# Optimization experiments

Measured on AMD Instinct MI355X. Metric: run time of the kernel, lower is better.

## Reference

```python
import jax, jax.numpy as jnp
import numpy as np

MAX_LORAS = 16
D_IN = 4096
D_OUT = 64
B = 32
S = 2048


def setup_inputs() -> dict:
    key = jax.random.key(0)
    k1, k2, k3 = jax.random.split(key, 3)
    x = jax.random.normal(k1, (B, S, D_IN), dtype=jnp.float32)
    adapter_ids = jax.random.randint(k2, (B,), 0, MAX_LORAS)
    # weight table: (max_loras, input_size, output_size) since memory_transpose=True
    weight = jax.random.normal(k3, (MAX_LORAS, D_IN, D_OUT), dtype=jnp.float32) * 0.02
    return {"x": x, "adapter_ids": adapter_ids, "weight": weight}


def reference(x, adapter_ids, weight):
    # get_weight: gather per-sample weight [B, D_IN, D_OUT]
    weights = weight[adapter_ids]
    # memory_transpose=True path: einsum('bij,bjk->bik')
    return jnp.einsum('bij,bjk->bik', x, weights)
```

## Files before the change

### kernel.cpp

```cpp
#include <hip/hip_runtime.h>

#define DIN 4096
#define DOUT 64
#define SEQ 2048
#define BK 64
#define WT_STRIDE 72

typedef __bf16 bf16x8 __attribute__((ext_vector_type(8)));
typedef float f32x4 __attribute__((ext_vector_type(4)));

__global__ __launch_bounds__(256, 2)
void lora_gemm_kernel(const float* __restrict__ x,
                      const int* __restrict__ adapter_ids,
                      const float* __restrict__ weight,
                      float* __restrict__ out)
{
    __shared__ __align__(16) __bf16 wt[64 * WT_STRIDE];

    const int bid  = blockIdx.x;
    const int row0 = bid * 64;
    const int b    = row0 / SEQ;
    const int aid  = adapter_ids[b];
    const float* wbase = weight + (size_t)aid * DIN * DOUT;

    const int tid  = threadIdx.x;
    const int wave = tid >> 6;
    const int lane = tid & 63;
    const int m16  = lane & 15;
    const int quad = lane >> 4;

    const float* xrow = x + (size_t)(row0 + wave * 16 + m16) * DIN + quad * 8;

    f32x4 acc[4];
#pragma unroll
    for (int t = 0; t < 4; ++t) acc[t] = (f32x4)0.0f;

    const int s_kk = tid >> 4;
    const int s_n4 = tid & 15;

    for (int k0 = 0; k0 < DIN; k0 += BK) {
#pragma unroll
        for (int p = 0; p < 4; ++p) {
            const int kk = p * 16 + s_kk;
            const f32x4 w4 = *(const f32x4*)(wbase + (size_t)(k0 + kk) * DOUT + s_n4 * 4);
#pragma unroll
            for (int i = 0; i < 4; ++i)
                wt[(s_n4 * 4 + i) * WT_STRIDE + kk] = (__bf16)w4[i];
        }
        __syncthreads();

#pragma unroll
        for (int ks = 0; ks < BK; ks += 32) {
            const f32x4 xa = *(const f32x4*)(xrow + k0 + ks);
            const f32x4 xb = *(const f32x4*)(xrow + k0 + ks + 4);
            bf16x8 a;
            a[0] = (__bf16)xa[0]; a[1] = (__bf16)xa[1];
            a[2] = (__bf16)xa[2]; a[3] = (__bf16)xa[3];
            a[4] = (__bf16)xb[0]; a[5] = (__bf16)xb[1];
            a[6] = (__bf16)xb[2]; a[7] = (__bf16)xb[3];
#pragma unroll
            for (int t = 0; t < 4; ++t) {
                const bf16x8 bf = *(const bf16x8*)(&wt[(t * 16 + m16) * WT_STRIDE + ks + quad * 8]);
                acc[t] = __builtin_amdgcn_mfma_f32_16x16x32_bf16(a, bf, acc[t], 0, 0, 0);
            }
        }
        __syncthreads();
    }

    float* obase = out + (size_t)(row0 + wave * 16 + quad * 4) * DOUT + m16;
#pragma unroll
    for (int i = 0; i < 4; ++i)
#pragma unroll
        for (int t = 0; t < 4; ++t)
            obase[(size_t)i * DOUT + t * 16] = acc[t][i];
}

extern "C" void kernel_launch(void* const* d_in, const int* in_sizes, int n_in,
                              void* d_out, int out_size, void* d_ws, size_t ws_size,
                              hipStream_t stream) {
    const float* x   = (const float*)d_in[0];
    const int*   ids = (const int*)d_in[1];
    const float* w   = (const float*)d_in[2];
    float* out = (float*)d_out;

    const int total_rows = 32 * SEQ;
    dim3 grid(total_rows / 64);
    dim3 block(256);
    lora_gemm_kernel<<<grid, block, 0, stream>>>(x, ids, w, out);
}
```

Before: 1.389 ms.

## Pre-transpose weights to bf16 and read B fragments directly from global

Adds a preprocessing kernel that converts all adapter weight tables to bf16 in an N-major (transposed) layout inside the workspace. The GEMM kernel then loads its B fragments straight from global/L2 memory, with no shared-memory staging and no __syncthreads per K tile, and occupancy is raised to 4 blocks per SM. This removes the per-block fp32 weight reload, conversion and LDS transpose, at the cost of an extra kernel launch and more global/L2 traffic for weight fragments.

New measurement: 1.499 ms. 1.08x slower.

```diff
diff --git a/kernel.cpp b/kernel.cpp
--- a/kernel.cpp
+++ b/kernel.cpp
@@ -3,25 +3,33 @@
 #define DIN 4096
 #define DOUT 64
 #define SEQ 2048
-#define BK 64
-#define WT_STRIDE 72
+#define NADPT 16
 
 typedef __bf16 bf16x8 __attribute__((ext_vector_type(8)));
 typedef float f32x4 __attribute__((ext_vector_type(4)));
 
-__global__ __launch_bounds__(256, 2)
+__global__ __launch_bounds__(256)
+void transpose_w_kernel(const float* __restrict__ w, __bf16* __restrict__ wT)
+{
+    const int a  = blockIdx.y;
+    const int k0 = blockIdx.x * 32 + (threadIdx.x >> 6) * 8;
+    const int n  = threadIdx.x & 63;
+    const float* src = w + ((size_t)a * DIN + k0) * DOUT + n;
+    bf16x8 v;
+#pragma unroll
+    for (int j = 0; j < 8; ++j)
+        v[j] = (__bf16)src[(size_t)j * DOUT];
+    *(bf16x8*)(wT + ((size_t)a * DOUT + n) * DIN + k0) = v;
+}
+
+__global__ __launch_bounds__(256, 4)
 void lora_gemm_kernel(const float* __restrict__ x,
                       const int* __restrict__ adapter_ids,
-                      const float* __restrict__ weight,
+                      const __bf16* __restrict__ wT,
                       float* __restrict__ out)
 {
-    __shared__ __align__(16) __bf16 wt[64 * WT_STRIDE];
-
-    const int bid  = blockIdx.x;
-    const int row0 = bid * 64;
-    const int b    = row0 / SEQ;
-    const int aid  = adapter_ids[b];
-    const float* wbase = weight + (size_t)aid * DIN * DOUT;
+    const int row0 = blockIdx.x * 64;
+    const int aid  = adapter_ids[row0 / SEQ];
 
     const int tid  = threadIdx.x;
     const int wave = tid >> 6;
@@ -29,42 +37,27 @@
     const int m16  = lane & 15;
     const int quad = lane >> 4;
 
-    const float* xrow = x + (size_t)(row0 + wave * 16 + m16) * DIN + quad * 8;
+    const float*  xrow = x  + (size_t)(row0 + wave * 16 + m16) * DIN + quad * 8;
+    const __bf16* wb   = wT + ((size_t)aid * DOUT + m16) * DIN + quad * 8;
 
     f32x4 acc[4];
 #pragma unroll
     for (int t = 0; t < 4; ++t) acc[t] = (f32x4)0.0f;
 
-    const int s_kk = tid >> 4;
-    const int s_n4 = tid & 15;
-
-    for (int k0 = 0; k0 < DIN; k0 += BK) {
+#pragma unroll 2
+    for (int k = 0; k < DIN; k += 32) {
+        const f32x4 xa = *(const f32x4*)(xrow + k);
+        const f32x4 xb = *(const f32x4*)(xrow + k + 4);
+        bf16x8 a;
+        a[0] = (__bf16)xa[0]; a[1] = (__bf16)xa[1];
+        a[2] = (__bf16)xa[2]; a[3] = (__bf16)xa[3];
+        a[4] = (__bf16)xb[0]; a[5] = (__bf16)xb[1];
+        a[6] = (__bf16)xb[2]; a[7] = (__bf16)xb[3];
 #pragma unroll
-        for (int p = 0; p < 4; ++p) {
-            const int kk = p * 16 + s_kk;
-            const f32x4 w4 = *(const f32x4*)(wbase + (size_t)(k0 + kk) * DOUT + s_n4 * 4);
-#pragma unroll
-            for (int i = 0; i < 4; ++i)
-                wt[(s_n4 * 4 + i) * WT_STRIDE + kk] = (__bf16)w4[i];
+        for (int t = 0; t < 4; ++t) {
+            const bf16x8 bf = *(const bf16x8*)(wb + (size_t)t * 16 * DIN + k);
+            acc[t] = __builtin_amdgcn_mfma_f32_16x16x32_bf16(a, bf, acc[t], 0, 0, 0);
         }
-        __syncthreads();
-
-#pragma unroll
-        for (int ks = 0; ks < BK; ks += 32) {
-            const f32x4 xa = *(const f32x4*)(xrow + k0 + ks);
-            const f32x4 xb = *(const f32x4*)(xrow + k0 + ks + 4);
-            bf16x8 a;
-            a[0] = (__bf16)xa[0]; a[1] = (__bf16)xa[1];
-            a[2] = (__bf16)xa[2]; a[3] = (__bf16)xa[3];
-            a[4] = (__bf16)xb[0]; a[5] = (__bf16)xb[1];
-            a[6] = (__bf16)xb[2]; a[7] = (__bf16)xb[3];
-#pragma unroll
-            for (int t = 0; t < 4; ++t) {
-                const bf16x8 bf = *(const bf16x8*)(&wt[(t * 16 + m16) * WT_STRIDE + ks + quad * 8]);
-                acc[t] = __builtin_amdgcn_mfma_f32_16x16x32_bf16(a, bf, acc[t], 0, 0, 0);
-            }
-        }
-        __syncthreads();
     }
 
     float* obase = out + (size_t)(row0 + wave * 16 + quad * 4) * DOUT + m16;
@@ -82,9 +75,11 @@
     const int*   ids = (const int*)d_in[1];
     const float* w   = (const float*)d_in[2];
     float* out = (float*)d_out;
+    __bf16* wT = (__bf16*)d_ws;
+
+    dim3 tgrid(DIN / 32, NADPT);
+    transpose_w_kernel<<<tgrid, 256, 0, stream>>>(w, wT);
 
     const int total_rows = 32 * SEQ;
-    dim3 grid(total_rows / 64);
-    dim3 block(256);
-    lora_gemm_kernel<<<grid, block, 0, stream>>>(x, ids, w, out);
+    lora_gemm_kernel<<<dim3(total_rows / 64), 256, 0, stream>>>(x, ids, wT, out);
 }
```
